# Kernel tuning notes

Measured on AMD Instinct MI355X. Metric: run time of the kernel, lower is better.

The kernel has to match this reference:

```python
import jax, jax.numpy as jnp
import numpy as np


def setup_inputs() -> dict:
    key = jax.random.key(0)
    B, C, H, W, A, G = 16, 512, 16, 16, 64, 256
    # Ragged group sizes (constant, deterministic) -> padded gather indices + mask
    rng = np.random.default_rng(0)
    sizes = rng.integers(32, 257, size=G)
    N = int(sizes.sum())          # ~36849 total sound tokens
    S_max = int(sizes.max())      # 256
    offsets = np.concatenate([[0], np.cumsum(sizes)[:-1]])
    pad_idx = np.zeros((G, S_max), dtype=np.int64)
    pad_mask = np.zeros((G, S_max), dtype=bool)
    for g in range(G):
        s = int(sizes[g])
        pad_idx[g, :s] = offsets[g] + np.arange(s)
        pad_mask[g, :s] = True
    k1, k2 = jax.random.split(key)
    return {
        'Z_img': jax.random.normal(k1, (B, C, H, W), jnp.float32),
        'Z_snd': jax.random.normal(k2, (N, C), jnp.float32),
        'pad_idx': jnp.asarray(pad_idx),
        'pad_mask': jnp.asarray(pad_mask),
        'attn_dims': A,
    }


def reference(Z_img, Z_snd, pad_idx, pad_mask, attn_dims):
    # Eval-mode forward of AudioAttention (no random subsampling).
    C = Z_img.shape[1]
    A = attn_dims
    # Global-average-pool image features: [B, C, H, W] -> [B, C]
    z = Z_img.reshape(Z_img.shape[0], C, -1).mean(axis=2)
    z_img, query = z[:, : C - A], z[:, C - A :]          # [B, C-A], [B, A]
    # Ragged groups as padded gather: [G, S, C]
    snd = Z_snd[pad_idx]
    value, key_ = snd[..., : C - A], snd[..., C - A :]   # [G,S,C-A], [G,S,A]
    # Per-group cross attention with the shared image queries
    scores = jnp.einsum('ba,gsa->gbs', query, key_)      # [G, B, S]
    scores = jnp.where(pad_mask[:, None, :], scores, -jnp.inf)
    attn = jax.nn.softmax(scores, axis=-1)               # padded cols -> 0 weight
    M_snd = jnp.einsum('gbs,gsc->gbc', attn, value)      # [G, B, C-A]
    M_img = jnp.broadcast_to(z_img[None], M_snd.shape)   # [G, B, C-A]
    return M_img, M_snd
```

## Files before the change

kernel.cpp:

```cpp
#include <hip/hip_runtime.h>
#include <math.h>

#define B_  16
#define C_  512
#define A_  64
#define CV  448
#define G_  256
#define HW  256
#define SMX 256
#define BSP 8

__global__ __launch_bounds__(256) void meanpool_kernel(const float* __restrict__ Zimg,
                                                       float* __restrict__ z) {
  int row  = (blockIdx.x << 2) + (threadIdx.x >> 6);
  int lane = threadIdx.x & 63;
  const float4* p = (const float4*)(Zimg + (size_t)row * HW);
  float4 v = p[lane];
  float s = (v.x + v.y) + (v.z + v.w);
  #pragma unroll
  for (int off = 32; off > 0; off >>= 1)
    s += __shfl_down(s, off, 64);
  if (lane == 0) z[row] = s * (1.0f / HW);
}

__global__ __launch_bounds__(512, 4) void fused_kernel(
    const float* __restrict__ Zsnd,
    const int*   __restrict__ pad_idx,
    const float* __restrict__ z,
    float*       __restrict__ Mimg,
    float*       __restrict__ Msnd,
    int Smax, int N)
{
  const int bid  = blockIdx.x;
  const int g    = bid & 255;
  const int bh   = bid >> 8;
  const int b0   = bh * BSP;
  const int t    = threadIdx.x;
  const int lane = t & 63;
  const int wave = t >> 6;

  __shared__ float qs[BSP * A_];
  __shared__ float attnT[SMX * BSP];
  __shared__ int   idxs[SMX];
  __shared__ float red[8 * BSP];
  __shared__ float red2[8 * BSP];
  __shared__ int   redi[8];
  __shared__ float redS[4 * BSP * 64 * 4];

  int sgv = 0;
  if (t < SMX) {
    int v = pad_idx[(size_t)g * Smax + t];
    bool ok = ((t == 0) || (v != 0)) && (v >= 0) && (v < N);
    idxs[t] = ok ? v : 0;
    sgv = ok ? (t + 1) : 0;
  }
  #pragma unroll
  for (int off = 32; off > 0; off >>= 1)
    sgv = max(sgv, __shfl_xor(sgv, off, 64));
  if (lane == 0) redi[wave] = sgv;

  if (t < BSP * 16) {
    int b = t >> 4, a4 = t & 15;
    *(float4*)(qs + b * A_ + a4 * 4) =
        *(const float4*)(z + (b0 + b) * C_ + CV + a4 * 4);
  }

  {
    int b = t >> 6, c = t & 63;
    float* mrow = Mimg + (size_t)g * (B_ * CV) + (b0 + b) * CV;
    const float* zrow = z + (b0 + b) * C_;
    *(float4*)(mrow + c * 4) = *(const float4*)(zrow + c * 4);
    int c2 = c + 64;
    if (c2 < 112)
      *(float4*)(mrow + c2 * 4) = *(const float4*)(zrow + c2 * 4);
  }

  __syncthreads();
  const int sg = max(max(max(redi[0], redi[1]), max(redi[2], redi[3])),
                     max(max(redi[4], redi[5]), max(redi[6], redi[7])));

  const int s_ = t >> 1;
  const int kh = t & 1;
  const bool valid = (s_ < sg);
  const float* krow = Zsnd + (size_t)idxs[s_] * C_ + CV + kh * 32;

  float sc[BSP];
  #pragma unroll
  for (int b = 0; b < BSP; b++) sc[b] = 0.0f;

  #pragma unroll
  for (int c = 0; c < 2; c++) {
    float4 k0 = *(const float4*)(krow + c * 16 + 0);
    float4 k1 = *(const float4*)(krow + c * 16 + 4);
    float4 k2 = *(const float4*)(krow + c * 16 + 8);
    float4 k3 = *(const float4*)(krow + c * 16 + 12);
    #pragma unroll
    for (int b = 0; b < BSP; b++) {
      const float* qb = qs + b * A_ + kh * 32 + c * 16;
      float4 q0 = *(const float4*)(qb + 0);
      float4 q1 = *(const float4*)(qb + 4);
      float4 q2 = *(const float4*)(qb + 8);
      float4 q3 = *(const float4*)(qb + 12);
      sc[b] += q0.x * k0.x + q0.y * k0.y + q0.z * k0.z + q0.w * k0.w
             + q1.x * k1.x + q1.y * k1.y + q1.z * k1.z + q1.w * k1.w
             + q2.x * k2.x + q2.y * k2.y + q2.z * k2.z + q2.w * k2.w
             + q3.x * k3.x + q3.y * k3.y + q3.z * k3.z + q3.w * k3.w;
    }
    __builtin_amdgcn_sched_barrier(0);
  }
  #pragma unroll
  for (int b = 0; b < BSP; b++)
    sc[b] += __shfl_xor(sc[b], 1, 64);

  #pragma unroll
  for (int b = 0; b < BSP; b++) {
    float v = valid ? sc[b] : -INFINITY;
    #pragma unroll
    for (int off = 32; off > 0; off >>= 1)
      v = fmaxf(v, __shfl_xor(v, off, 64));
    if (lane == 0) red[wave * BSP + b] = v;
  }
  __syncthreads();

  float ex[BSP];
  #pragma unroll
  for (int b = 0; b < BSP; b++) {
    float gm = red[0 * BSP + b];
    #pragma unroll
    for (int w2 = 1; w2 < 8; w2++) gm = fmaxf(gm, red[w2 * BSP + b]);
    float e = valid ? __expf(sc[b] - gm) : 0.0f;
    ex[b] = e;
    float es = (kh == 0) ? e : 0.0f;
    #pragma unroll
    for (int off = 32; off > 0; off >>= 1)
      es += __shfl_xor(es, off, 64);
    if (lane == 0) red2[wave * BSP + b] = es;
  }
  __syncthreads();

  if (kh == 0) {
    float iv[BSP];
    #pragma unroll
    for (int b = 0; b < BSP; b++) {
      float gs = red2[0 * BSP + b];
      #pragma unroll
      for (int w2 = 1; w2 < 8; w2++) gs += red2[w2 * BSP + b];
      iv[b] = ex[b] / gs;
    }
    *(float4*)(attnT + s_ * BSP + 0) = make_float4(iv[0], iv[1], iv[2], iv[3]);
    *(float4*)(attnT + s_ * BSP + 4) = make_float4(iv[4], iv[5], iv[6], iv[7]);
  }
  __syncthreads();

  const int ch = wave >> 1;
  const int sh = wave & 1;
  const int cl = lane & 31;
  const int h  = lane >> 5;
  const int c0 = ch * 128;
  const int sg32 = (sg + 31) & ~31;

  const float* vbase = Zsnd + c0 + cl * 4;
  float4 acc[BSP];
  #pragma unroll
  for (int b = 0; b < BSP; b++) acc[b] = make_float4(0.f, 0.f, 0.f, 0.f);

  for (int s0 = 0; s0 < sg32; s0 += 32) {
    float4 v[8];
    #pragma unroll
    for (int j = 0; j < 8; j++) {
      int so = s0 + 4 * j + 2 * sh + h;
      v[j] = *(const float4*)(vbase + (size_t)idxs[so] * C_);
    }
    #pragma unroll
    for (int j = 0; j < 8; j++) {
      int so = s0 + 4 * j + 2 * sh + h;
      float4 w0 = *(const float4*)(attnT + so * BSP + 0);
      float4 w1 = *(const float4*)(attnT + so * BSP + 4);
      float4 vv = v[j];
      acc[0].x += w0.x * vv.x; acc[0].y += w0.x * vv.y; acc[0].z += w0.x * vv.z; acc[0].w += w0.x * vv.w;
      acc[1].x += w0.y * vv.x; acc[1].y += w0.y * vv.y; acc[1].z += w0.y * vv.z; acc[1].w += w0.y * vv.w;
      acc[2].x += w0.z * vv.x; acc[2].y += w0.z * vv.y; acc[2].z += w0.z * vv.z; acc[2].w += w0.z * vv.w;
      acc[3].x += w0.w * vv.x; acc[3].y += w0.w * vv.y; acc[3].z += w0.w * vv.z; acc[3].w += w0.w * vv.w;
      acc[4].x += w1.x * vv.x; acc[4].y += w1.x * vv.y; acc[4].z += w1.x * vv.z; acc[4].w += w1.x * vv.w;
      acc[5].x += w1.y * vv.x; acc[5].y += w1.y * vv.y; acc[5].z += w1.y * vv.z; acc[5].w += w1.y * vv.w;
      acc[6].x += w1.z * vv.x; acc[6].y += w1.z * vv.y; acc[6].z += w1.z * vv.z; acc[6].w += w1.z * vv.w;
      acc[7].x += w1.w * vv.x; acc[7].y += w1.w * vv.y; acc[7].z += w1.w * vv.z; acc[7].w += w1.w * vv.w;
    }
  }

  if (sh == 1) {
    #pragma unroll
    for (int b = 0; b < BSP; b++)
      *(float4*)(redS + (((size_t)ch * BSP + b) * 64 + lane) * 4) = acc[b];
  }
  __syncthreads();
  if (sh == 0) {
    #pragma unroll
    for (int b = 0; b < BSP; b++) {
      float4 o = *(const float4*)(redS + (((size_t)ch * BSP + b) * 64 + lane) * 4);
      acc[b].x += o.x; acc[b].y += o.y; acc[b].z += o.z; acc[b].w += o.w;
      acc[b].x += __shfl_xor(acc[b].x, 32, 64);
      acc[b].y += __shfl_xor(acc[b].y, 32, 64);
      acc[b].z += __shfl_xor(acc[b].z, 32, 64);
      acc[b].w += __shfl_xor(acc[b].w, 32, 64);
    }
    if (h == 0 && c0 + cl * 4 < CV) {
      float* obase = Msnd + (size_t)g * (B_ * CV) + (size_t)b0 * CV + c0 + cl * 4;
      #pragma unroll
      for (int b = 0; b < BSP; b++)
        *(float4*)(obase + b * CV) = acc[b];
    }
  }
}

extern "C" void kernel_launch(void* const* d_in, const int* in_sizes, int n_in,
                              void* d_out, int out_size, void* d_ws, size_t ws_size,
                              hipStream_t stream) {
  const float* Zimg   = (const float*)d_in[0];
  const float* Zsnd   = (const float*)d_in[1];
  const int*   padidx = (const int*)d_in[2];

  const int N    = in_sizes[1] / C_;
  const int Smax = in_sizes[2] / G_;

  float* z    = (float*)d_ws;
  float* Mimg = (float*)d_out;
  float* Msnd = Mimg + (size_t)G_ * B_ * CV;

  meanpool_kernel<<<(B_ * C_) / 4, 256, 0, stream>>>(Zimg, z);
  fused_kernel<<<G_ * 2, 512, 0, stream>>>(Zsnd, padidx, z, Mimg, Msnd, Smax, N);
}
```

Measured before the change: 154.5 us.

## Split fused attention into score, stats and sliced PV kernels with atomics

Replaces the single fused per-group kernel with three kernels. The first computes scores per 64-row slice for all 16 batch rows. The second computes per-group softmax max and sum and also writes M_img. The third applies the softmax weights per slice and accumulates into a pre-zeroed M_snd through atomicAdd. The aim is more parallelism, about 2048 blocks of 256 threads, and skipping fully padded slices. The cost is extra launches, a round trip of the scores through global memory, and many float atomics.

Result: slower. 207.9 us (+34.6%).

```diff
diff --git a/kernel.cpp b/kernel.cpp
--- a/kernel.cpp
+++ b/kernel.cpp
@@ -8,12 +8,17 @@
 #define G_  256
 #define HW  256
 #define SMX 256
-#define BSP 8
+#define SLICE 64
+#define NSL  4
 
 __global__ __launch_bounds__(256) void meanpool_kernel(const float* __restrict__ Zimg,
-                                                       float* __restrict__ z) {
-  int row  = (blockIdx.x << 2) + (threadIdx.x >> 6);
-  int lane = threadIdx.x & 63;
+                                                       float* __restrict__ z,
+                                                       float* __restrict__ Msnd) {
+  const int bid = blockIdx.x, t = threadIdx.x;
+  if (t < 224)
+    *(float4*)(Msnd + (size_t)bid * 896 + t * 4) = make_float4(0.f, 0.f, 0.f, 0.f);
+  int row  = (bid << 2) + (t >> 6);
+  int lane = t & 63;
   const float4* p = (const float4*)(Zimg + (size_t)row * HW);
   float4 v = p[lane];
   float s = (v.x + v.y) + (v.z + v.w);
@@ -23,159 +28,198 @@
   if (lane == 0) z[row] = s * (1.0f / HW);
 }
 
-__global__ __launch_bounds__(512, 4) void fused_kernel(
+__global__ __launch_bounds__(256, 4) void score_kernel(
     const float* __restrict__ Zsnd,
     const int*   __restrict__ pad_idx,
     const float* __restrict__ z,
-    float*       __restrict__ Mimg,
-    float*       __restrict__ Msnd,
+    float*       __restrict__ scores,
     int Smax, int N)
 {
-  const int bid  = blockIdx.x;
-  const int g    = bid & 255;
-  const int bh   = bid >> 8;
-  const int b0   = bh * BSP;
-  const int t    = threadIdx.x;
-  const int lane = t & 63;
-  const int wave = t >> 6;
-
-  __shared__ float qs[BSP * A_];
-  __shared__ float attnT[SMX * BSP];
-  __shared__ int   idxs[SMX];
-  __shared__ float red[8 * BSP];
-  __shared__ float red2[8 * BSP];
-  __shared__ int   redi[8];
-  __shared__ float redS[4 * BSP * 64 * 4];
-
-  int sgv = 0;
-  if (t < SMX) {
-    int v = pad_idx[(size_t)g * Smax + t];
-    bool ok = ((t == 0) || (v != 0)) && (v >= 0) && (v < N);
-    idxs[t] = ok ? v : 0;
-    sgv = ok ? (t + 1) : 0;
-  }
-  #pragma unroll
-  for (int off = 32; off > 0; off >>= 1)
-    sgv = max(sgv, __shfl_xor(sgv, off, 64));
-  if (lane == 0) redi[wave] = sgv;
-
-  if (t < BSP * 16) {
-    int b = t >> 4, a4 = t & 15;
+  const int bid = blockIdx.x;
+  const int g   = bid >> 2;
+  const int s0  = (bid & 3) * SLICE;
+  const int t   = threadIdx.x;
+
+  __shared__ float qs[B_ * A_];
+  __shared__ int   idx[SLICE];
+
+  if (t < SLICE) {
+    int s = s0 + t;
+    int v = (s < Smax) ? pad_idx[(size_t)g * Smax + s] : 0;
+    bool ok = (s < Smax) && ((s == 0) || (v != 0)) && (v >= 0) && (v < N);
+    idx[t] = ok ? v : -1;
+  }
+  { int b = t >> 4, a4 = t & 15;
     *(float4*)(qs + b * A_ + a4 * 4) =
-        *(const float4*)(z + (b0 + b) * C_ + CV + a4 * 4);
-  }
-
-  {
-    int b = t >> 6, c = t & 63;
-    float* mrow = Mimg + (size_t)g * (B_ * CV) + (b0 + b) * CV;
-    const float* zrow = z + (b0 + b) * C_;
-    *(float4*)(mrow + c * 4) = *(const float4*)(zrow + c * 4);
-    int c2 = c + 64;
-    if (c2 < 112)
-      *(float4*)(mrow + c2 * 4) = *(const float4*)(zrow + c2 * 4);
-  }
-
-  __syncthreads();
-  const int sg = max(max(max(redi[0], redi[1]), max(redi[2], redi[3])),
-                     max(max(redi[4], redi[5]), max(redi[6], redi[7])));
-
-  const int s_ = t >> 1;
-  const int kh = t & 1;
-  const bool valid = (s_ < sg);
-  const float* krow = Zsnd + (size_t)idxs[s_] * C_ + CV + kh * 32;
-
-  float sc[BSP];
-  #pragma unroll
-  for (int b = 0; b < BSP; b++) sc[b] = 0.0f;
-
-  #pragma unroll
-  for (int c = 0; c < 2; c++) {
-    float4 k0 = *(const float4*)(krow + c * 16 + 0);
-    float4 k1 = *(const float4*)(krow + c * 16 + 4);
-    float4 k2 = *(const float4*)(krow + c * 16 + 8);
-    float4 k3 = *(const float4*)(krow + c * 16 + 12);
-    #pragma unroll
-    for (int b = 0; b < BSP; b++) {
-      const float* qb = qs + b * A_ + kh * 32 + c * 16;
+        *(const float4*)(z + b * C_ + CV + a4 * 4); }
+  __syncthreads();
+
+  const int s_l = t >> 2, kq = t & 3;
+  const int my  = idx[s_l];
+
+  float sc[B_];
+  #pragma unroll
+  for (int b = 0; b < B_; b++) sc[b] = 0.0f;
+
+  if (my >= 0) {
+    const float* kr = Zsnd + (size_t)my * C_ + CV + kq * 16;
+    float4 k0 = *(const float4*)(kr + 0);
+    float4 k1 = *(const float4*)(kr + 4);
+    float4 k2 = *(const float4*)(kr + 8);
+    float4 k3 = *(const float4*)(kr + 12);
+    #pragma unroll
+    for (int b = 0; b < B_; b++) {
+      const float* qb = qs + b * A_ + kq * 16;
       float4 q0 = *(const float4*)(qb + 0);
       float4 q1 = *(const float4*)(qb + 4);
       float4 q2 = *(const float4*)(qb + 8);
       float4 q3 = *(const float4*)(qb + 12);
-      sc[b] += q0.x * k0.x + q0.y * k0.y + q0.z * k0.z + q0.w * k0.w
-             + q1.x * k1.x + q1.y * k1.y + q1.z * k1.z + q1.w * k1.w
-             + q2.x * k2.x + q2.y * k2.y + q2.z * k2.z + q2.w * k2.w
-             + q3.x * k3.x + q3.y * k3.y + q3.z * k3.z + q3.w * k3.w;
-    }
-    __builtin_amdgcn_sched_barrier(0);
-  }
-  #pragma unroll
-  for (int b = 0; b < BSP; b++)
+      sc[b] = q0.x * k0.x + q0.y * k0.y + q0.z * k0.z + q0.w * k0.w
+            + q1.x * k1.x + q1.y * k1.y + q1.z * k1.z + q1.w * k1.w
+            + q2.x * k2.x + q2.y * k2.y + q2.z * k2.z + q2.w * k2.w
+            + q3.x * k3.x + q3.y * k3.y + q3.z * k3.z + q3.w * k3.w;
+    }
+  }
+  #pragma unroll
+  for (int b = 0; b < B_; b++) {
     sc[b] += __shfl_xor(sc[b], 1, 64);
-
-  #pragma unroll
-  for (int b = 0; b < BSP; b++) {
-    float v = valid ? sc[b] : -INFINITY;
+    sc[b] += __shfl_xor(sc[b], 2, 64);
+  }
+  if (kq == 0) {
+    float* out = scores + ((size_t)g * SMX + s0 + s_l) * B_;
+    if (my >= 0) {
+      *(float4*)(out + 0)  = make_float4(sc[0],  sc[1],  sc[2],  sc[3]);
+      *(float4*)(out + 4)  = make_float4(sc[4],  sc[5],  sc[6],  sc[7]);
+      *(float4*)(out + 8)  = make_float4(sc[8],  sc[9],  sc[10], sc[11]);
+      *(float4*)(out + 12) = make_float4(sc[12], sc[13], sc[14], sc[15]);
+    } else {
+      float4 ninf = make_float4(-INFINITY, -INFINITY, -INFINITY, -INFINITY);
+      *(float4*)(out + 0) = ninf; *(float4*)(out + 4) = ninf;
+      *(float4*)(out + 8) = ninf; *(float4*)(out + 12) = ninf;
+    }
+  }
+}
+
+__global__ __launch_bounds__(256) void stats_kernel(
+    const float* __restrict__ scores,
+    const float* __restrict__ z,
+    float*       __restrict__ m_g,
+    float*       __restrict__ l_g,
+    float*       __restrict__ Mimg)
+{
+  const int g = blockIdx.x, t = threadIdx.x, lane = t & 63, wave = t >> 6;
+  __shared__ float red[4][B_];
+  __shared__ float red2[4][B_];
+
+  const float* srow = scores + ((size_t)g * SMX + t) * B_;
+  float sc[B_];
+  #pragma unroll
+  for (int i = 0; i < 4; i++) {
+    float4 v = *(const float4*)(srow + i * 4);
+    sc[i * 4 + 0] = v.x; sc[i * 4 + 1] = v.y; sc[i * 4 + 2] = v.z; sc[i * 4 + 3] = v.w;
+  }
+  #pragma unroll
+  for (int b = 0; b < B_; b++) {
+    float v = sc[b];
     #pragma unroll
     for (int off = 32; off > 0; off >>= 1)
       v = fmaxf(v, __shfl_xor(v, off, 64));
-    if (lane == 0) red[wave * BSP + b] = v;
-  }
-  __syncthreads();
-
-  float ex[BSP];
-  #pragma unroll
-  for (int b = 0; b < BSP; b++) {
-    float gm = red[0 * BSP + b];
-    #pragma unroll
-    for (int w2 = 1; w2 < 8; w2++) gm = fmaxf(gm, red[w2 * BSP + b]);
-    float e = valid ? __expf(sc[b] - gm) : 0.0f;
-    ex[b] = e;
-    float es = (kh == 0) ? e : 0.0f;
+    if (lane == 0) red[wave][b] = v;
+  }
+  __syncthreads();
+  #pragma unroll
+  for (int b = 0; b < B_; b++) {
+    float gm = fmaxf(fmaxf(red[0][b], red[1][b]), fmaxf(red[2][b], red[3][b]));
+    float e  = __expf(sc[b] - gm);
     #pragma unroll
     for (int off = 32; off > 0; off >>= 1)
-      es += __shfl_xor(es, off, 64);
-    if (lane == 0) red2[wave * BSP + b] = es;
-  }
-  __syncthreads();
-
-  if (kh == 0) {
-    float iv[BSP];
-    #pragma unroll
-    for (int b = 0; b < BSP; b++) {
-      float gs = red2[0 * BSP + b];
-      #pragma unroll
-      for (int w2 = 1; w2 < 8; w2++) gs += red2[w2 * BSP + b];
-      iv[b] = ex[b] / gs;
-    }
-    *(float4*)(attnT + s_ * BSP + 0) = make_float4(iv[0], iv[1], iv[2], iv[3]);
-    *(float4*)(attnT + s_ * BSP + 4) = make_float4(iv[4], iv[5], iv[6], iv[7]);
-  }
-  __syncthreads();
-
-  const int ch = wave >> 1;
-  const int sh = wave & 1;
+      e += __shfl_xor(e, off, 64);
+    if (lane == 0) red2[wave][b] = e;
+  }
+  __syncthreads();
+  if (t < B_) {
+    float gm = fmaxf(fmaxf(red[0][t], red[1][t]), fmaxf(red[2][t], red[3][t]));
+    float gs = (red2[0][t] + red2[1][t]) + (red2[2][t] + red2[3][t]);
+    m_g[g * B_ + t] = gm;
+    l_g[g * B_ + t] = gs;
+  }
+  #pragma unroll
+  for (int i = 0; i < 7; i++) {
+    int li = i * 256 + t;
+    int b = li / 112, c4 = li % 112;
+    *(float4*)(Mimg + (size_t)g * (B_ * CV) + b * CV + c4 * 4) =
+        *(const float4*)(z + b * C_ + c4 * 4);
+  }
+}
+
+__global__ __launch_bounds__(256, 4) void pv_kernel(
+    const float* __restrict__ Zsnd,
+    const int*   __restrict__ pad_idx,
+    const float* __restrict__ scores,
+    const float* __restrict__ m_g,
+    const float* __restrict__ l_g,
+    float*       __restrict__ Msnd,
+    int Smax, int N)
+{
+  const int bid = blockIdx.x;
+  const int bh  = bid >> 10;
+  const int r   = bid & 1023;
+  const int g   = r >> 2;
+  const int s0  = (r & 3) * SLICE;
+  const int b0  = bh * 8;
+  const int t    = threadIdx.x;
+  const int lane = t & 63;
+  const int wave = t >> 6;
+
+  __shared__ int   idx[SLICE];
+  __shared__ float w[SLICE][8];
+  __shared__ float mls[16];
+
+  if (t < SLICE) {
+    int s = s0 + t;
+    int v = (s < Smax) ? pad_idx[(size_t)g * Smax + s] : 0;
+    bool ok = (s < Smax) && ((s == 0) || (v != 0)) && (v >= 0) && (v < N);
+    idx[t] = ok ? v : -1;
+  }
+  if (t < 8) {
+    mls[t]     = m_g[g * B_ + b0 + t];
+    mls[8 + t] = 1.0f / l_g[g * B_ + b0 + t];
+  }
+  __syncthreads();
+  if (idx[0] < 0) return;
+
+  {
+    const int s_l = t & 63, bq = t >> 6;
+    const float2 s2 = *(const float2*)(scores + ((size_t)g * SMX + s0 + s_l) * B_ + b0 + bq * 2);
+    w[s_l][bq * 2 + 0] = __expf(s2.x - mls[bq * 2 + 0]) * mls[8 + bq * 2 + 0];
+    w[s_l][bq * 2 + 1] = __expf(s2.y - mls[bq * 2 + 1]) * mls[8 + bq * 2 + 1];
+    if (t < SLICE && idx[t] < 0) idx[t] = 0;
+  }
+  __syncthreads();
+
+  const int ch = wave;
   const int cl = lane & 31;
   const int h  = lane >> 5;
   const int c0 = ch * 128;
-  const int sg32 = (sg + 31) & ~31;
 
   const float* vbase = Zsnd + c0 + cl * 4;
-  float4 acc[BSP];
-  #pragma unroll
-  for (int b = 0; b < BSP; b++) acc[b] = make_float4(0.f, 0.f, 0.f, 0.f);
-
-  for (int s0 = 0; s0 < sg32; s0 += 32) {
+  float4 acc[8];
+  #pragma unroll
+  for (int b = 0; b < 8; b++) acc[b] = make_float4(0.f, 0.f, 0.f, 0.f);
+
+  #pragma unroll
+  for (int it = 0; it < 4; it++) {
     float4 v[8];
     #pragma unroll
     for (int j = 0; j < 8; j++) {
-      int so = s0 + 4 * j + 2 * sh + h;
-      v[j] = *(const float4*)(vbase + (size_t)idxs[so] * C_);
+      int s_l = it * 16 + j * 2 + h;
+      v[j] = *(const float4*)(vbase + (size_t)idx[s_l] * C_);
     }
     #pragma unroll
     for (int j = 0; j < 8; j++) {
-      int so = s0 + 4 * j + 2 * sh + h;
-      float4 w0 = *(const float4*)(attnT + so * BSP + 0);
-      float4 w1 = *(const float4*)(attnT + so * BSP + 4);
+      int s_l = it * 16 + j * 2 + h;
+      float4 w0 = *(const float4*)(&w[s_l][0]);
+      float4 w1 = *(const float4*)(&w[s_l][4]);
       float4 vv = v[j];
       acc[0].x += w0.x * vv.x; acc[0].y += w0.x * vv.y; acc[0].z += w0.x * vv.z; acc[0].w += w0.x * vv.w;
       acc[1].x += w0.y * vv.x; acc[1].y += w0.y * vv.y; acc[1].z += w0.y * vv.z; acc[1].w += w0.y * vv.w;
@@ -188,27 +232,21 @@
     }
   }
 
-  if (sh == 1) {
-    #pragma unroll
-    for (int b = 0; b < BSP; b++)
-      *(float4*)(redS + (((size_t)ch * BSP + b) * 64 + lane) * 4) = acc[b];
-  }
-  __syncthreads();
-  if (sh == 0) {
-    #pragma unroll
-    for (int b = 0; b < BSP; b++) {
-      float4 o = *(const float4*)(redS + (((size_t)ch * BSP + b) * 64 + lane) * 4);
-      acc[b].x += o.x; acc[b].y += o.y; acc[b].z += o.z; acc[b].w += o.w;
-      acc[b].x += __shfl_xor(acc[b].x, 32, 64);
-      acc[b].y += __shfl_xor(acc[b].y, 32, 64);
-      acc[b].z += __shfl_xor(acc[b].z, 32, 64);
-      acc[b].w += __shfl_xor(acc[b].w, 32, 64);
-    }
-    if (h == 0 && c0 + cl * 4 < CV) {
-      float* obase = Msnd + (size_t)g * (B_ * CV) + (size_t)b0 * CV + c0 + cl * 4;
-      #pragma unroll
-      for (int b = 0; b < BSP; b++)
-        *(float4*)(obase + b * CV) = acc[b];
+  #pragma unroll
+  for (int b = 0; b < 8; b++) {
+    acc[b].x += __shfl_xor(acc[b].x, 32, 64);
+    acc[b].y += __shfl_xor(acc[b].y, 32, 64);
+    acc[b].z += __shfl_xor(acc[b].z, 32, 64);
+    acc[b].w += __shfl_xor(acc[b].w, 32, 64);
+  }
+  if (h == 0 && c0 + cl * 4 < CV) {
+    float* ob = Msnd + (size_t)g * (B_ * CV) + (size_t)b0 * CV + c0 + cl * 4;
+    #pragma unroll
+    for (int b = 0; b < 8; b++) {
+      atomicAdd(ob + b * CV + 0, acc[b].x);
+      atomicAdd(ob + b * CV + 1, acc[b].y);
+      atomicAdd(ob + b * CV + 2, acc[b].z);
+      atomicAdd(ob + b * CV + 3, acc[b].w);
     }
   }
 }
@@ -223,10 +261,15 @@
   const int N    = in_sizes[1] / C_;
   const int Smax = in_sizes[2] / G_;
 
-  float* z    = (float*)d_ws;
+  float* z      = (float*)d_ws;
+  float* scores = z + B_ * C_;
+  float* m_g    = scores + (size_t)G_ * SMX * B_;
+  float* l_g    = m_g + G_ * B_;
   float* Mimg = (float*)d_out;
   float* Msnd = Mimg + (size_t)G_ * B_ * CV;
 
-  meanpool_kernel<<<(B_ * C_) / 4, 256, 0, stream>>>(Zimg, z);
-  fused_kernel<<<G_ * 2, 512, 0, stream>>>(Zsnd, padidx, z, Mimg, Msnd, Smax, N);
-}
+  meanpool_kernel<<<(B_ * C_) / 4, 256, 0, stream>>>(Zimg, z, Msnd);
+  score_kernel<<<G_ * NSL, 256, 0, stream>>>(Zsnd, padidx, z, scores, Smax, N);
+  stats_kernel<<<G_, 256, 0, stream>>>(scores, z, m_g, l_g, Mimg);
+  pv_kernel<<<G_ * NSL * 2, 256, 0, stream>>>(Zsnd, padidx, scores, m_g, l_g, Msnd, Smax, N);
+}
```

## Schedule ragged groups longest-first via precomputed sizes and skip invalid key loads

Applied to the files above, without the earlier changes.

The meanpool kernel now also computes each group's valid length. A new single-block kernel bucket-sorts the groups by length into a rank array, and the fused kernel reads that array so larger groups are dispatched first. The block mapping also pairs ranks from both ends of the order across the two batch halves. Score computation is now skipped for rows beyond the group length. The aim is to reduce tail imbalance from ragged groups, at the cost of an extra tiny kernel launch and a serial dependency.

New measurement: 184.4 us. 19.4% more time.

```diff
diff --git a/kernel.cpp b/kernel.cpp
--- a/kernel.cpp
+++ b/kernel.cpp
@@ -11,9 +11,27 @@
 #define BSP 8
 
 __global__ __launch_bounds__(256) void meanpool_kernel(const float* __restrict__ Zimg,
-                                                       float* __restrict__ z) {
-  int row  = (blockIdx.x << 2) + (threadIdx.x >> 6);
-  int lane = threadIdx.x & 63;
+                                                       float* __restrict__ z,
+                                                       const int* __restrict__ pad_idx,
+                                                       int* __restrict__ sgArr,
+                                                       int Smax, int N) {
+  const int bid = blockIdx.x, t = threadIdx.x;
+  const int lane = t & 63, wave = t >> 6;
+  __shared__ int r4[4];
+
+  if (bid < G_) {
+    int v = pad_idx[(size_t)bid * Smax + t];
+    bool ok = ((t == 0) || (v != 0)) && (v >= 0) && (v < N);
+    int sgv = ok ? (t + 1) : 0;
+    #pragma unroll
+    for (int off = 32; off > 0; off >>= 1)
+      sgv = max(sgv, __shfl_xor(sgv, off, 64));
+    if (lane == 0) r4[wave] = sgv;
+    __syncthreads();
+    if (t == 0) sgArr[bid] = max(max(r4[0], r4[1]), max(r4[2], r4[3]));
+  }
+
+  int row = (bid << 2) + (t >> 6);
   const float4* p = (const float4*)(Zimg + (size_t)row * HW);
   float4 v = p[lane];
   float s = (v.x + v.y) + (v.z + v.w);
@@ -21,19 +39,40 @@
   for (int off = 32; off > 0; off >>= 1)
     s += __shfl_down(s, off, 64);
   if (lane == 0) z[row] = s * (1.0f / HW);
+}
+
+__global__ __launch_bounds__(256) void sched_kernel(const int* __restrict__ sgArr,
+                                                    int* __restrict__ grank) {
+  __shared__ int cnt[8], base[8];
+  const int t = threadIdx.x;
+  if (t < 8) cnt[t] = 0;
+  __syncthreads();
+  int sg = sgArr[t];
+  int bk = min(7, max(0, sg - 32) >> 5);
+  atomicAdd(&cnt[bk], 1);
+  __syncthreads();
+  if (t == 0) {
+    int o = 0;
+    for (int b = 7; b >= 0; b--) { base[b] = o; o += cnt[b]; }
+  }
+  __syncthreads();
+  int r = atomicAdd(&base[bk], 1);
+  grank[r] = t;
 }
 
 __global__ __launch_bounds__(512, 4) void fused_kernel(
     const float* __restrict__ Zsnd,
     const int*   __restrict__ pad_idx,
     const float* __restrict__ z,
+    const int*   __restrict__ grank,
     float*       __restrict__ Mimg,
     float*       __restrict__ Msnd,
     int Smax, int N)
 {
   const int bid  = blockIdx.x;
-  const int g    = bid & 255;
-  const int bh   = bid >> 8;
+  const int p_   = bid & 127;
+  const int bh   = (bid >> 7) & 1;
+  const int g    = (bid >> 8) ? grank[255 - p_] : grank[p_];
   const int b0   = bh * BSP;
   const int t    = threadIdx.x;
   const int lane = t & 63;
@@ -88,25 +127,27 @@
   #pragma unroll
   for (int b = 0; b < BSP; b++) sc[b] = 0.0f;
 
-  #pragma unroll
-  for (int c = 0; c < 2; c++) {
-    float4 k0 = *(const float4*)(krow + c * 16 + 0);
-    float4 k1 = *(const float4*)(krow + c * 16 + 4);
-    float4 k2 = *(const float4*)(krow + c * 16 + 8);
-    float4 k3 = *(const float4*)(krow + c * 16 + 12);
-    #pragma unroll
-    for (int b = 0; b < BSP; b++) {
-      const float* qb = qs + b * A_ + kh * 32 + c * 16;
-      float4 q0 = *(const float4*)(qb + 0);
-      float4 q1 = *(const float4*)(qb + 4);
-      float4 q2 = *(const float4*)(qb + 8);
-      float4 q3 = *(const float4*)(qb + 12);
-      sc[b] += q0.x * k0.x + q0.y * k0.y + q0.z * k0.z + q0.w * k0.w
-             + q1.x * k1.x + q1.y * k1.y + q1.z * k1.z + q1.w * k1.w
-             + q2.x * k2.x + q2.y * k2.y + q2.z * k2.z + q2.w * k2.w
-             + q3.x * k3.x + q3.y * k3.y + q3.z * k3.z + q3.w * k3.w;
-    }
-    __builtin_amdgcn_sched_barrier(0);
+  if (valid) {
+    #pragma unroll
+    for (int c = 0; c < 2; c++) {
+      float4 k0 = *(const float4*)(krow + c * 16 + 0);
+      float4 k1 = *(const float4*)(krow + c * 16 + 4);
+      float4 k2 = *(const float4*)(krow + c * 16 + 8);
+      float4 k3 = *(const float4*)(krow + c * 16 + 12);
+      #pragma unroll
+      for (int b = 0; b < BSP; b++) {
+        const float* qb = qs + b * A_ + kh * 32 + c * 16;
+        float4 q0 = *(const float4*)(qb + 0);
+        float4 q1 = *(const float4*)(qb + 4);
+        float4 q2 = *(const float4*)(qb + 8);
+        float4 q3 = *(const float4*)(qb + 12);
+        sc[b] += q0.x * k0.x + q0.y * k0.y + q0.z * k0.z + q0.w * k0.w
+               + q1.x * k1.x + q1.y * k1.y + q1.z * k1.z + q1.w * k1.w
+               + q2.x * k2.x + q2.y * k2.y + q2.z * k2.z + q2.w * k2.w
+               + q3.x * k3.x + q3.y * k3.y + q3.z * k3.z + q3.w * k3.w;
+      }
+      __builtin_amdgcn_sched_barrier(0);
+    }
   }
   #pragma unroll
   for (int b = 0; b < BSP; b++)
@@ -223,10 +264,13 @@
   const int N    = in_sizes[1] / C_;
   const int Smax = in_sizes[2] / G_;
 
-  float* z    = (float*)d_ws;
+  float* z     = (float*)d_ws;
+  int*   sgArr = (int*)(z + B_ * C_);
+  int*   grank = sgArr + G_;
   float* Mimg = (float*)d_out;
   float* Msnd = Mimg + (size_t)G_ * B_ * CV;
 
-  meanpool_kernel<<<(B_ * C_) / 4, 256, 0, stream>>>(Zimg, z);
-  fused_kernel<<<G_ * 2, 512, 0, stream>>>(Zsnd, padidx, z, Mimg, Msnd, Smax, N);
-}
+  meanpool_kernel<<<(B_ * C_) / 4, 256, 0, stream>>>(Zimg, z, padidx, sgArr, Smax, N);
+  sched_kernel<<<1, 256, 0, stream>>>(sgArr, grank);
+  fused_kernel<<<G_ * 2, 512, 0, stream>>>(Zsnd, padidx, z, grank, Mimg, Msnd, Smax, N);
+}
```
